# Performance work log

Measured on AMD Instinct MI355X. Metric: run time of the kernel, lower is better.

## Reference

```python
import jax, jax.numpy as jnp
import numpy as np


def setup_inputs() -> dict:
    key = jax.random.key(0)
    B, D = 8192, 4096
    ks = jax.random.split(key, 6)
    s = 1.0 / np.sqrt(D)  # nn.init.uniform_(-1/sqrt(D), 1/sqrt(D))
    return {
        "u": jax.random.normal(ks[0], (B, D), dtype=jnp.float32),
        "w1": jax.random.uniform(ks[1], (D,), jnp.float32, -s, s),
        "w2": jax.random.uniform(ks[2], (D,), jnp.float32, -s, s),
        "w3": jax.random.uniform(ks[3], (D,), jnp.float32, -s, s),
        "bias1": jnp.ones((1,), jnp.float32),
        "bias2": jnp.ones((1,), jnp.float32),
        # nn.Linear(D, 1): kaiming-uniform-ish init approximated with same bound
        "delta_w": jax.random.uniform(ks[4], (1, D), jnp.float32, -s, s),
        "delta_b": jax.random.uniform(ks[5], (1,), jnp.float32, -s, s),
    }


def reference(u, w1, w2, w3, bias1, bias2, delta_w, delta_b):
    # select = softplus(delta(u) + bias1), shape [B]
    select = jax.nn.softplus(u @ delta_w.T + delta_b + bias1)[:, 0]
    # einsum('bi,b->b', M, x) == (sum_i M[b,i]) * x[b], so the recurrence
    # collapses to scalar-per-batch coefficients:
    a = select * (u @ w1)   # sum_i Abar[b,i] = select[b] * sum_i w1[i]*u[b,i]
    b = u @ w2              # sum_i Bbar[b,i]
    c = u @ w3              # sum_i Cbar[b,i]
    Dc = bias2[0]
    ut = u.T                # [T, B], time-major for scan; T == input_dim
    x0 = b * ut[0]          # xi at step 0; y[:,0] = x0 (no C/D term in original)

    def step(x, ui):
        xn = a * x + b * ui
        return xn, c * xn + Dc * ui

    _, ys = jax.lax.scan(step, x0, ut[1:])  # ys: [T-1, B]
    y = jnp.concatenate([x0[None, :], ys], axis=0).T  # [B, T]
    return y
```

## Files before the change

kernel.cpp:

```cpp
#include <hip/hip_runtime.h>
#include <math.h>


#define DDIM 4096

__device__ __forceinline__ float clf_always(float v) {
    int b   = __float_as_int(v);
    int mag = b & 0x7fffffff;
    if (mag >= 0x7F7A0000)
        v = __int_as_float((b & 0x80000000) | 0x7F7A0000);
    return v;
}

template <bool CL>
__device__ __forceinline__ float cl(float v) {
    if (CL) return clf_always(v);
    return v;
}

__device__ __forceinline__ float softplus_ref(float z) {
    return (z > 0.0f) ? (z + log1pf(expf(-z))) : log1pf(expf(z));
}

template <bool CL>
__device__ __forceinline__ void phase2(
    int tid, int wid, int lane,
    const float4* uv, float* wt,
    float a, float bb, float cc, float Dc,
    float r1, float r2, float r4, float r8, float r16, float r32,
    float a256, float a1024, float P,
    float* __restrict__ yrow)
{
    float Bv[4];
#pragma unroll
    for (int j = 0; j < 4; ++j) {
        float B = bb * uv[j].x;
        B = fmaf(a, B, bb * uv[j].y);
        B = fmaf(a, B, bb * uv[j].z);
        B = fmaf(a, B, bb * uv[j].w);
        Bv[j] = cl<CL>(B);
    }

#pragma unroll
    for (int j = 0; j < 4; ++j) {
        float B = Bv[j];
        float t;
        t = __shfl_up(B, 1,  64); if (lane >= 1)  B = cl<CL>(fmaf(r1,  t, B));
        t = __shfl_up(B, 2,  64); if (lane >= 2)  B = cl<CL>(fmaf(r2,  t, B));
        t = __shfl_up(B, 4,  64); if (lane >= 4)  B = cl<CL>(fmaf(r4,  t, B));
        t = __shfl_up(B, 8,  64); if (lane >= 8)  B = cl<CL>(fmaf(r8,  t, B));
        t = __shfl_up(B, 16, 64); if (lane >= 16) B = cl<CL>(fmaf(r16, t, B));
        t = __shfl_up(B, 32, 64); if (lane >= 32) B = cl<CL>(fmaf(r32, t, B));
        Bv[j] = B;
    }

    float T[4];
#pragma unroll
    for (int j = 0; j < 4; ++j) T[j] = __shfl(Bv[j], 63, 64);

    float W = T[0];
    W = cl<CL>(fmaf(a256, W, T[1]));
    W = cl<CL>(fmaf(a256, W, T[2]));
    W = cl<CL>(fmaf(a256, W, T[3]));
    if (lane == 0) wt[wid] = W;
    __syncthreads();

    float cr = 0.0f;
    for (int w = 0; w < wid; ++w) cr = cl<CL>(fmaf(a1024, cr, wt[w]));

#pragma unroll
    for (int j = 0; j < 4; ++j) {
        const int idx = (wid * 4 + j) * 256 + lane * 4;
        float Cprev = __shfl_up(Bv[j], 1, 64);
        if (lane == 0) Cprev = 0.0f;

        const float xs = cl<CL>(fmaf(P, cr, Cprev));
        const float x0 = cl<CL>(fmaf(a, xs, bb * uv[j].x));
        const float x1 = cl<CL>(fmaf(a, x0, bb * uv[j].y));
        const float x2 = cl<CL>(fmaf(a, x1, bb * uv[j].z));
        const float x3 = cl<CL>(fmaf(a, x2, bb * uv[j].w));

        float4 yv;
        yv.x = cl<CL>(fmaf(cc, x0, Dc * uv[j].x));
        yv.y = cl<CL>(fmaf(cc, x1, Dc * uv[j].y));
        yv.z = cl<CL>(fmaf(cc, x2, Dc * uv[j].z));
        yv.w = cl<CL>(fmaf(cc, x3, Dc * uv[j].w));
        if (j == 0 && tid == 0) yv.x = x0;
        *reinterpret_cast<float4*>(yrow + idx) = yv;

        cr = cl<CL>(fmaf(a256, cr, T[j]));
    }
}

__global__ __launch_bounds__(256) void ssm_kernel(
    const float* __restrict__ u,
    const float* __restrict__ w1,
    const float* __restrict__ w2,
    const float* __restrict__ w3,
    const float* __restrict__ bias1,
    const float* __restrict__ bias2,
    const float* __restrict__ dw,
    const float* __restrict__ db,
    float* __restrict__ y)
{
    const int tid  = threadIdx.x;
    const int wid  = tid >> 6;
    const int lane = tid & 63;
    const int row  = blockIdx.x;

    const float* __restrict__ urow = u + (size_t)row * DDIM;
    float* __restrict__ yrow       = y + (size_t)row * DDIM;

    __shared__ float4 red[4];
    __shared__ float  wt[4];

    float4 uv[4];
    float s0 = 0.f, s1 = 0.f, s2 = 0.f, s3 = 0.f;
#pragma unroll
    for (int j = 0; j < 4; ++j) {
        const int idx = (wid * 4 + j) * 256 + lane * 4;
        uv[j] = *reinterpret_cast<const float4*>(urow + idx);
        const float4 dv = *reinterpret_cast<const float4*>(dw + idx);
        const float4 a1 = *reinterpret_cast<const float4*>(w1 + idx);
        const float4 a2 = *reinterpret_cast<const float4*>(w2 + idx);
        const float4 a3 = *reinterpret_cast<const float4*>(w3 + idx);
        s0 += uv[j].x * dv.x + uv[j].y * dv.y + uv[j].z * dv.z + uv[j].w * dv.w;
        s1 += uv[j].x * a1.x + uv[j].y * a1.y + uv[j].z * a1.z + uv[j].w * a1.w;
        s2 += uv[j].x * a2.x + uv[j].y * a2.y + uv[j].z * a2.z + uv[j].w * a2.w;
        s3 += uv[j].x * a3.x + uv[j].y * a3.y + uv[j].z * a3.z + uv[j].w * a3.w;
    }
#pragma unroll
    for (int d = 1; d < 64; d <<= 1) {
        s0 += __shfl_xor(s0, d, 64);
        s1 += __shfl_xor(s1, d, 64);
        s2 += __shfl_xor(s2, d, 64);
        s3 += __shfl_xor(s3, d, 64);
    }
    if (lane == 0) red[wid] = make_float4(s0, s1, s2, s3);
    __syncthreads();
    {
        const float4 p0 = red[0], p1 = red[1], p2 = red[2], p3 = red[3];
        s0 = p0.x + p1.x + p2.x + p3.x;
        s1 = p0.y + p1.y + p2.y + p3.y;
        s2 = p0.z + p1.z + p2.z + p3.z;
        s3 = p0.w + p1.w + p2.w + p3.w;
    }

    const float sel = softplus_ref(s0 + db[0] + bias1[0]);
    const float a   = clf_always(sel * s1);
    const float bb  = s2;
    const float cc  = s3;
    const float Dc  = bias2[0];

    const bool fast = (fabsf(a) <= 1.015f);

    if (fast) {
        const float a2p   = a * a;
        const float r1    = a2p * a2p;
        const float r2    = r1 * r1;
        const float r4    = r2 * r2;
        const float r8    = r4 * r4;
        const float r16   = r8 * r8;
        const float r32   = r16 * r16;
        const float a256  = r32 * r32;
        const float a1024 = (a256 * a256) * (a256 * a256);
        float P = 1.0f;
        if (lane & 1)  P *= r1;
        if (lane & 2)  P *= r2;
        if (lane & 4)  P *= r4;
        if (lane & 8)  P *= r8;
        if (lane & 16) P *= r16;
        if (lane & 32) P *= r32;
        phase2<false>(tid, wid, lane, uv, wt, a, bb, cc, Dc,
                      r1, r2, r4, r8, r16, r32, a256, a1024, P, yrow);
    } else {
        const float a2p   = clf_always(a * a);
        const float r1    = clf_always(a2p * a2p);
        const float r2    = clf_always(r1 * r1);
        const float r4    = clf_always(r2 * r2);
        const float r8    = clf_always(r4 * r4);
        const float r16   = clf_always(r8 * r8);
        const float r32   = clf_always(r16 * r16);
        const float a256  = clf_always(r32 * r32);
        const float a1024 = clf_always(clf_always(a256 * a256) * clf_always(a256 * a256));
        float P = 1.0f;
        if (lane & 1)  P = clf_always(P * r1);
        if (lane & 2)  P = clf_always(P * r2);
        if (lane & 4)  P = clf_always(P * r4);
        if (lane & 8)  P = clf_always(P * r8);
        if (lane & 16) P = clf_always(P * r16);
        if (lane & 32) P = clf_always(P * r32);
        phase2<true>(tid, wid, lane, uv, wt, a, bb, cc, Dc,
                     r1, r2, r4, r8, r16, r32, a256, a1024, P, yrow);
    }
}

extern "C" void kernel_launch(void* const* d_in, const int* in_sizes, int n_in,
                              void* d_out, int out_size, void* d_ws, size_t ws_size,
                              hipStream_t stream) {
    const float* u     = (const float*)d_in[0];
    const float* w1    = (const float*)d_in[1];
    const float* w2    = (const float*)d_in[2];
    const float* w3    = (const float*)d_in[3];
    const float* bias1 = (const float*)d_in[4];
    const float* bias2 = (const float*)d_in[5];
    const float* dw    = (const float*)d_in[6];
    const float* db    = (const float*)d_in[7];
    float* y = (float*)d_out;

    const int B = in_sizes[0] / DDIM;
    dim3 grid(B), block(256);
    hipLaunchKernelGGL(ssm_kernel, grid, block, 0, stream,
                       u, w1, w2, w3, bias1, bias2, dw, db, y);
}
```

Baseline: 248.9 us.

## Split fused SSM kernel into separate dot-product and scan kernels

Splits the single kernel into two. The first computes the four per-row dot products with one wavefront per row, so it needs no block-wide reduction or barrier, and stores the coefficients in a workspace. The second reloads each row of u and runs the scan using those coefficients. The goal is to remove the block reduction and barrier from the scan kernel and shrink per-kernel work, at the cost of reading u twice from memory and an extra kernel launch.

```diff
diff --git a/kernel.cpp b/kernel.cpp
--- a/kernel.cpp
+++ b/kernel.cpp
@@ -22,15 +22,74 @@
     return (z > 0.0f) ? (z + log1pf(expf(-z))) : log1pf(expf(z));
 }
 
+__global__ __launch_bounds__(256) void ssm_dots(
+    const float* __restrict__ u,
+    const float* __restrict__ w1,
+    const float* __restrict__ w2,
+    const float* __restrict__ w3,
+    const float* __restrict__ bias1,
+    const float* __restrict__ dw,
+    const float* __restrict__ db,
+    float4* __restrict__ coef)
+{
+    const int wid  = threadIdx.x >> 6;
+    const int lane = threadIdx.x & 63;
+    const int row  = (blockIdx.x << 2) + wid;
+
+    const float* __restrict__ urow = u + (size_t)row * DDIM;
+
+    float s0 = 0.f, s1 = 0.f, s2 = 0.f, s3 = 0.f;
+#pragma unroll 4
+    for (int it = 0; it < 16; ++it) {
+        const int idx = it * 256 + lane * 4;
+        const float4 uv = *reinterpret_cast<const float4*>(urow + idx);
+        const float4 dv = *reinterpret_cast<const float4*>(dw + idx);
+        const float4 a1 = *reinterpret_cast<const float4*>(w1 + idx);
+        const float4 a2 = *reinterpret_cast<const float4*>(w2 + idx);
+        const float4 a3 = *reinterpret_cast<const float4*>(w3 + idx);
+        s0 += uv.x * dv.x + uv.y * dv.y + uv.z * dv.z + uv.w * dv.w;
+        s1 += uv.x * a1.x + uv.y * a1.y + uv.z * a1.z + uv.w * a1.w;
+        s2 += uv.x * a2.x + uv.y * a2.y + uv.z * a2.z + uv.w * a2.w;
+        s3 += uv.x * a3.x + uv.y * a3.y + uv.z * a3.z + uv.w * a3.w;
+    }
+#pragma unroll
+    for (int d = 1; d < 64; d <<= 1) {
+        s0 += __shfl_xor(s0, d, 64);
+        s1 += __shfl_xor(s1, d, 64);
+        s2 += __shfl_xor(s2, d, 64);
+        s3 += __shfl_xor(s3, d, 64);
+    }
+    if (lane == 0) {
+        const float sel = softplus_ref(s0 + db[0] + bias1[0]);
+        const float a   = clf_always(sel * s1);
+        coef[row] = make_float4(a, s2, s3, 0.0f);
+    }
+}
+
 template <bool CL>
-__device__ __forceinline__ void phase2(
+__device__ __forceinline__ void scan_body(
     int tid, int wid, int lane,
     const float4* uv, float* wt,
     float a, float bb, float cc, float Dc,
-    float r1, float r2, float r4, float r8, float r16, float r32,
-    float a256, float a1024, float P,
     float* __restrict__ yrow)
 {
+    const float a2p   = cl<CL>(a * a);
+    const float r1    = cl<CL>(a2p * a2p);
+    const float r2    = cl<CL>(r1 * r1);
+    const float r4    = cl<CL>(r2 * r2);
+    const float r8    = cl<CL>(r4 * r4);
+    const float r16   = cl<CL>(r8 * r8);
+    const float r32   = cl<CL>(r16 * r16);
+    const float a256  = cl<CL>(r32 * r32);
+    const float a1024 = cl<CL>(cl<CL>(a256 * a256) * cl<CL>(a256 * a256));
+    float P = 1.0f;
+    if (lane & 1)  P = cl<CL>(P * r1);
+    if (lane & 2)  P = cl<CL>(P * r2);
+    if (lane & 4)  P = cl<CL>(P * r4);
+    if (lane & 8)  P = cl<CL>(P * r8);
+    if (lane & 16) P = cl<CL>(P * r16);
+    if (lane & 32) P = cl<CL>(P * r32);
+
     float Bv[4];
 #pragma unroll
     for (int j = 0; j < 4; ++j) {
@@ -92,15 +151,10 @@
     }
 }
 
-__global__ __launch_bounds__(256) void ssm_kernel(
+__global__ __launch_bounds__(256) void ssm_scan(
     const float* __restrict__ u,
-    const float* __restrict__ w1,
-    const float* __restrict__ w2,
-    const float* __restrict__ w3,
-    const float* __restrict__ bias1,
+    const float4* __restrict__ coef,
     const float* __restrict__ bias2,
-    const float* __restrict__ dw,
-    const float* __restrict__ db,
     float* __restrict__ y)
 {
     const int tid  = threadIdx.x;
@@ -111,87 +165,24 @@
     const float* __restrict__ urow = u + (size_t)row * DDIM;
     float* __restrict__ yrow       = y + (size_t)row * DDIM;
 
-    __shared__ float4 red[4];
-    __shared__ float  wt[4];
+    __shared__ float wt[4];
 
     float4 uv[4];
-    float s0 = 0.f, s1 = 0.f, s2 = 0.f, s3 = 0.f;
 #pragma unroll
     for (int j = 0; j < 4; ++j) {
         const int idx = (wid * 4 + j) * 256 + lane * 4;
         uv[j] = *reinterpret_cast<const float4*>(urow + idx);
-        const float4 dv = *reinterpret_cast<const float4*>(dw + idx);
-        const float4 a1 = *reinterpret_cast<const float4*>(w1 + idx);
-        const float4 a2 = *reinterpret_cast<const float4*>(w2 + idx);
-        const float4 a3 = *reinterpret_cast<const float4*>(w3 + idx);
-        s0 += uv[j].x * dv.x + uv[j].y * dv.y + uv[j].z * dv.z + uv[j].w * dv.w;
-        s1 += uv[j].x * a1.x + uv[j].y * a1.y + uv[j].z * a1.z + uv[j].w * a1.w;
-        s2 += uv[j].x * a2.x + uv[j].y * a2.y + uv[j].z * a2.z + uv[j].w * a2.w;
-        s3 += uv[j].x * a3.x + uv[j].y * a3.y + uv[j].z * a3.z + uv[j].w * a3.w;
-    }
-#pragma unroll
-    for (int d = 1; d < 64; d <<= 1) {
-        s0 += __shfl_xor(s0, d, 64);
-        s1 += __shfl_xor(s1, d, 64);
-        s2 += __shfl_xor(s2, d, 64);
-        s3 += __shfl_xor(s3, d, 64);
-    }
-    if (lane == 0) red[wid] = make_float4(s0, s1, s2, s3);
-    __syncthreads();
-    {
-        const float4 p0 = red[0], p1 = red[1], p2 = red[2], p3 = red[3];
-        s0 = p0.x + p1.x + p2.x + p3.x;
-        s1 = p0.y + p1.y + p2.y + p3.y;
-        s2 = p0.z + p1.z + p2.z + p3.z;
-        s3 = p0.w + p1.w + p2.w + p3.w;
-    }
-
-    const float sel = softplus_ref(s0 + db[0] + bias1[0]);
-    const float a   = clf_always(sel * s1);
-    const float bb  = s2;
-    const float cc  = s3;
-    const float Dc  = bias2[0];
-
-    const bool fast = (fabsf(a) <= 1.015f);
-
-    if (fast) {
-        const float a2p   = a * a;
-        const float r1    = a2p * a2p;
-        const float r2    = r1 * r1;
-        const float r4    = r2 * r2;
-        const float r8    = r4 * r4;
-        const float r16   = r8 * r8;
-        const float r32   = r16 * r16;
-        const float a256  = r32 * r32;
-        const float a1024 = (a256 * a256) * (a256 * a256);
-        float P = 1.0f;
-        if (lane & 1)  P *= r1;
-        if (lane & 2)  P *= r2;
-        if (lane & 4)  P *= r4;
-        if (lane & 8)  P *= r8;
-        if (lane & 16) P *= r16;
-        if (lane & 32) P *= r32;
-        phase2<false>(tid, wid, lane, uv, wt, a, bb, cc, Dc,
-                      r1, r2, r4, r8, r16, r32, a256, a1024, P, yrow);
+    }
+    const float4 cf = coef[row];
+    const float a  = cf.x;
+    const float bb = cf.y;
+    const float cc = cf.z;
+    const float Dc = bias2[0];
+
+    if (fabsf(a) <= 1.015f) {
+        scan_body<false>(tid, wid, lane, uv, wt, a, bb, cc, Dc, yrow);
     } else {
-        const float a2p   = clf_always(a * a);
-        const float r1    = clf_always(a2p * a2p);
-        const float r2    = clf_always(r1 * r1);
-        const float r4    = clf_always(r2 * r2);
-        const float r8    = clf_always(r4 * r4);
-        const float r16   = clf_always(r8 * r8);
-        const float r32   = clf_always(r16 * r16);
-        const float a256  = clf_always(r32 * r32);
-        const float a1024 = clf_always(clf_always(a256 * a256) * clf_always(a256 * a256));
-        float P = 1.0f;
-        if (lane & 1)  P = clf_always(P * r1);
-        if (lane & 2)  P = clf_always(P * r2);
-        if (lane & 4)  P = clf_always(P * r4);
-        if (lane & 8)  P = clf_always(P * r8);
-        if (lane & 16) P = clf_always(P * r16);
-        if (lane & 32) P = clf_always(P * r32);
-        phase2<true>(tid, wid, lane, uv, wt, a, bb, cc, Dc,
-                     r1, r2, r4, r8, r16, r32, a256, a1024, P, yrow);
+        scan_body<true>(tid, wid, lane, uv, wt, a, bb, cc, Dc, yrow);
     }
 }
 
@@ -206,10 +197,16 @@
     const float* bias2 = (const float*)d_in[5];
     const float* dw    = (const float*)d_in[6];
     const float* db    = (const float*)d_in[7];
-    float* y = (float*)d_out;
+    float* y      = (float*)d_out;
+    float4* coef  = (float4*)d_ws;
 
     const int B = in_sizes[0] / DDIM;
-    dim3 grid(B), block(256);
-    hipLaunchKernelGGL(ssm_kernel, grid, block, 0, stream,
-                       u, w1, w2, w3, bias1, bias2, dw, db, y);
-}
+
+    dim3 gridA(B / 4), blockA(256);
+    hipLaunchKernelGGL(ssm_dots, gridA, blockA, 0, stream,
+                       u, w1, w2, w3, bias1, dw, db, coef);
+
+    dim3 gridB(B), blockB(256);
+    hipLaunchKernelGGL(ssm_scan, gridB, blockB, 0, stream,
+                       u, coef, bias2, y);
+}
```

Result: slower. 266.8 us (+7.2%).
